# Kernel tuning notes

Hardware: AMD Instinct MI355X
Metric: run time of the kernel (lower is better)

## Reference

```python
import jax, jax.numpy as jnp
import numpy as np

N_FEAT = 350; D = 512; L = 4; DS = 64; NREG = 6; REG_E = 32
B = 32; S = 2048
CLAMP = 20.0


def _ln(x, g, b, eps=1e-5):
    mu = jnp.mean(x, axis=-1, keepdims=True)
    var = jnp.mean(jnp.square(x - mu), axis=-1, keepdims=True)
    return (x - mu) * jax.lax.rsqrt(var + eps) * g + b


def _slstm(x, ln_g, ln_b, Wi, bi, Wf, bf, Wz, bz, Wo, bo, Wp, bp):
    # x: [B,S,D] -> out: [B,S,D]
    xn = _ln(x, ln_g, ln_b)
    log_i = jnp.clip(jnp.einsum('bsd,de->bse', xn, Wi) + bi, -CLAMP, CLAMP)
    log_f = jnp.clip(jnp.einsum('bsd,de->bse', xn, Wf) + bf, -CLAMP, CLAMP)
    z = jnp.tanh(jnp.einsum('bsd,de->bse', xn, Wz) + bz)
    o = jax.nn.sigmoid(jnp.einsum('bsd,de->bse', xn, Wo) + bo)

    def step(carry, inp):
        m, c = carry
        li, lf, zt, ot = inp
        m_new = jnp.maximum(m + lf, li)
        i_s = jnp.exp(li - m_new)
        f_s = jnp.exp(m + lf - m_new)
        c_new = f_s * c + i_s * zt
        h = ot * jnp.tanh(c_new)
        return (m_new, c_new), h

    bsz = x.shape[0]
    init = (jnp.zeros((bsz, DS), x.dtype), jnp.zeros((bsz, DS), x.dtype))
    seq = (jnp.swapaxes(log_i, 0, 1), jnp.swapaxes(log_f, 0, 1),
           jnp.swapaxes(z, 0, 1), jnp.swapaxes(o, 0, 1))
    _, hs = jax.lax.scan(step, init, seq)  # hs: [S,B,DS]
    hs = jnp.swapaxes(hs, 0, 1)  # [B,S,DS]
    return jnp.einsum('bse,ed->bsd', hs, Wp) + bp


def setup_inputs() -> dict:
    key = jax.random.key(0)
    ks = iter(jax.random.split(key, 64))
    def p(*shape):
        return jax.random.normal(next(ks), shape, dtype=jnp.float32) * 0.02
    return {
        'x': jax.random.normal(next(ks), (B, S, N_FEAT), dtype=jnp.float32),
        'regime_ids': jax.random.randint(next(ks), (B, S), 0, NREG),
        'emb_regime': p(NREG, REG_E),
        'grn_w1': p(N_FEAT + REG_E, D), 'grn_b1': jnp.zeros((D,), jnp.float32),
        'grn_w2': p(D, N_FEAT), 'grn_b2': jnp.zeros((N_FEAT,), jnp.float32),
        'in_w': p(N_FEAT, D), 'in_b': jnp.zeros((D,), jnp.float32),
        'ln_in_g': jnp.ones((L, D), jnp.float32), 'ln_in_b': jnp.zeros((L, D), jnp.float32),
        'wi': p(L, D, DS), 'bi': jnp.zeros((L, DS), jnp.float32),
        'wf': p(L, D, DS), 'bf': jnp.zeros((L, DS), jnp.float32),
        'wz': p(L, D, DS), 'bz': jnp.zeros((L, DS), jnp.float32),
        'wo': p(L, D, DS), 'bo': jnp.zeros((L, DS), jnp.float32),
        'wp': p(L, DS, D), 'bp': jnp.zeros((L, D), jnp.float32),
        'nm_g': jnp.ones((L, D), jnp.float32), 'nm_b': jnp.zeros((L, D), jnp.float32),
        'hd15_w': p(D, 1), 'hd15_b': jnp.zeros((1,), jnp.float32),
        'hd30_w': p(D, 1), 'hd30_b': jnp.zeros((1,), jnp.float32),
        'hv_w': p(D, 3), 'hv_b': jnp.zeros((3,), jnp.float32),
        'hreg_w': p(D, NREG), 'hreg_b': jnp.zeros((NREG,), jnp.float32),
        'hrng_w': p(D, 3), 'hrng_b': jnp.zeros((3,), jnp.float32),
    }


def reference(x, regime_ids, emb_regime, grn_w1, grn_b1, grn_w2, grn_b2,
              in_w, in_b, ln_in_g, ln_in_b, wi, bi, wf, bf, wz, bz, wo, bo,
              wp, bp, nm_g, nm_b, hd15_w, hd15_b, hd30_w, hd30_b,
              hv_w, hv_b, hreg_w, hreg_b, hrng_w, hrng_b):
    # Variable selection network (regime-conditioned feature weights)
    remb = emb_regime[regime_ids]                      # [B,S,32]
    comb = jnp.concatenate([x, remb], axis=-1)         # [B,S,382]
    hidden = jax.nn.elu(jnp.einsum('bsf,fd->bsd', comb, grn_w1) + grn_b1)
    weights = jax.nn.softmax(jnp.einsum('bsd,df->bsf', hidden, grn_w2) + grn_b2, axis=-1)
    xw = x * weights
    h = jnp.einsum('bsf,fd->bsd', xw, in_w) + in_b     # [B,S,D]
    for l in range(L):
        res = _slstm(h, ln_in_g[l], ln_in_b[l], wi[l], bi[l], wf[l], bf[l],
                     wz[l], bz[l], wo[l], bo[l], wp[l], bp[l])
        h = _ln(h + res, nm_g[l], nm_b[l])
    h_last = h[:, -1, :]
    return (jnp.squeeze(h_last @ hd15_w + hd15_b, -1),
            jnp.squeeze(h_last @ hd30_w + hd30_b, -1),
            h_last @ hv_w + hv_b,
            h_last @ hreg_w + hreg_b,
            h_last @ hrng_w + hrng_b,
            h_last,
            weights[:, -1, :])
```

## Files before the change

kernel.cpp:

```cpp
#include <hip/hip_runtime.h>
#include <cmath>

#define NFEAT 350
#define DMODEL 512
#define NLAYER 4
#define DSZ 64
#define REG_E 32
#define BATCH 32
#define SEQ 2048
#define MTOK (BATCH * SEQ)
#define CLAMP_V 20.0f

#define CHUNK 64
#define NCHUNK (SEQ / CHUNK)

typedef short bf16x8 __attribute__((ext_vector_type(8)));
typedef float f32x4 __attribute__((ext_vector_type(4)));

__device__ __forceinline__ unsigned short f2b(float v) {
    union { float f; unsigned int u; } x; x.f = v;
    unsigned int r = x.u + 0x7fffu + ((x.u >> 16) & 1u);
    return (unsigned short)(r >> 16);
}
__device__ __forceinline__ float b2f(unsigned short u) {
    union { unsigned int i; float f; } x; x.i = ((unsigned int)u) << 16;
    return x.f;
}
__device__ __forceinline__ unsigned int pack2(float a, float b) {
    return ((unsigned int)f2b(b) << 16) | f2b(a);
}

__global__ __launch_bounds__(256) void tconv_k(const float* __restrict__ src,
                                               unsigned short* __restrict__ dst,
                                               int K, int N, int Kpad) {
    int k = blockIdx.x * 256 + threadIdx.x;
    int n = blockIdx.y;
    if (k >= Kpad) return;
    float v = (k < K && n < N) ? src[(size_t)k * N + n] : 0.f;
    dst[(size_t)n * Kpad + k] = f2b(v);
}

__global__ __launch_bounds__(256) void tconv_g_k(const float* __restrict__ wi,
                                                 const float* __restrict__ wf,
                                                 const float* __restrict__ wz,
                                                 const float* __restrict__ wo,
                                                 unsigned short* __restrict__ dst) {
    int k = blockIdx.x * 256 + threadIdx.x;
    int n = blockIdx.y;
    int z = blockIdx.z;
    int l = z >> 2, g = z & 3;
    const float* src = (g == 0 ? wi : g == 1 ? wf : g == 2 ? wz : wo) + (size_t)l * DMODEL * DSZ;
    dst[(size_t)z * 32768 + (size_t)n * 512 + k] = f2b(src[(size_t)k * DSZ + n]);
}

__global__ __launch_bounds__(1024) void gbias_k(const float* bi, const float* bf_,
                                                const float* bz, const float* bo,
                                                float* __restrict__ gbias) {
    int t = threadIdx.x;
    int l = t >> 8, r = t & 255, g = r >> 6, e = r & 63;
    const float* s = (g == 0 ? bi : g == 1 ? bf_ : g == 2 ? bz : bo);
    gbias[t] = s[l * 64 + e];
}

__global__ __launch_bounds__(256) void build_xc_k(const float* __restrict__ x,
                                                  const int* __restrict__ rid,
                                                  const float* __restrict__ emb,
                                                  unsigned short* __restrict__ xc) {
    int i = blockIdx.x * 256 + threadIdx.x;
    int m = i / 192, p = i - m * 192;
    int k = p * 2;
    float a = 0.f, b = 0.f;
    if (k < 350) {
        const float2 v = *(const float2*)(x + (size_t)m * NFEAT + k);
        a = v.x; b = v.y;
    } else if (k < 382) {
        int r = rid[m];
        const float2 v = *(const float2*)(emb + r * REG_E + (k - 350));
        a = v.x; b = v.y;
    }
    ((unsigned int*)xc)[(size_t)m * 192 + p] = pack2(a, b);
}

template <int ALD, int EPI>
__global__ __launch_bounds__(256) void mgemm_k(const unsigned short* __restrict__ Ab,
                                               const float* __restrict__ Af,
                                               const unsigned short* __restrict__ Bt,
                                               const float* __restrict__ bias,
                                               float* __restrict__ Cf,
                                               unsigned short* __restrict__ Cb,
                                               const float* __restrict__ muA,
                                               const float* __restrict__ rstdA,
                                               const float* __restrict__ lng,
                                               const float* __restrict__ lnb,
                                               float* __restrict__ statS,
                                               float* __restrict__ statQ,
                                               int lda, int ldb, int K, int N, int ldc) {
    __shared__ unsigned short As[128][40];
    __shared__ unsigned short Bs[128][40];
    const int tid = threadIdx.x;
    const int lane = tid & 63;
    const int wave = tid >> 6;
    const int l15 = lane & 15;
    const int quad = lane >> 4;
    const int wm = (wave >> 1) * 64;
    const int wn = (wave & 1) * 64;
    const size_t m0 = (size_t)blockIdx.y * 128;
    const int n0 = blockIdx.x * 128;

    const int sr = tid >> 2;
    const int ku = tid & 3;

    const unsigned short* Br0 = Bt + ((size_t)(n0 + sr)) * ldb + ku * 8;
    const unsigned short* Br1 = Br0 + (size_t)64 * ldb;

    const unsigned short* Ar0 = nullptr;
    const unsigned short* Ar1 = nullptr;
    const float* Fr0 = nullptr;
    const float* Fr1 = nullptr;
    float mu0 = 0.f, rs0 = 0.f, mu1 = 0.f, rs1 = 0.f;
    if (ALD == 0) {
        Ar0 = Ab + (m0 + sr) * (size_t)lda + ku * 8;
        Ar1 = Ar0 + (size_t)64 * lda;
    } else {
        Fr0 = Af + (m0 + sr) * (size_t)lda + ku * 8;
        Fr1 = Fr0 + (size_t)64 * lda;
        mu0 = muA[m0 + sr];   rs0 = rstdA[m0 + sr];
        mu1 = muA[m0 + sr + 64]; rs1 = rstdA[m0 + sr + 64];
    }

    f32x4 acc[4][4] = {};

    for (int k0 = 0; k0 < K; k0 += 32) {
        if (ALD == 0) {
            *(uint4*)&As[sr][ku * 8]      = *(const uint4*)(Ar0 + k0);
            *(uint4*)&As[sr + 64][ku * 8] = *(const uint4*)(Ar1 + k0);
        } else {
            float4 g0 = *(const float4*)(lng + k0 + ku * 8);
            float4 g1 = *(const float4*)(lng + k0 + ku * 8 + 4);
            float4 c0 = *(const float4*)(lnb + k0 + ku * 8);
            float4 c1 = *(const float4*)(lnb + k0 + ku * 8 + 4);
            {
                float4 v0 = *(const float4*)(Fr0 + k0);
                float4 v1 = *(const float4*)(Fr0 + k0 + 4);
                uint4 w;
                w.x = pack2((v0.x - mu0) * rs0 * g0.x + c0.x, (v0.y - mu0) * rs0 * g0.y + c0.y);
                w.y = pack2((v0.z - mu0) * rs0 * g0.z + c0.z, (v0.w - mu0) * rs0 * g0.w + c0.w);
                w.z = pack2((v1.x - mu0) * rs0 * g1.x + c1.x, (v1.y - mu0) * rs0 * g1.y + c1.y);
                w.w = pack2((v1.z - mu0) * rs0 * g1.z + c1.z, (v1.w - mu0) * rs0 * g1.w + c1.w);
                *(uint4*)&As[sr][ku * 8] = w;
            }
            {
                float4 v0 = *(const float4*)(Fr1 + k0);
                float4 v1 = *(const float4*)(Fr1 + k0 + 4);
                uint4 w;
                w.x = pack2((v0.x - mu1) * rs1 * g0.x + c0.x, (v0.y - mu1) * rs1 * g0.y + c0.y);
                w.y = pack2((v0.z - mu1) * rs1 * g0.z + c0.z, (v0.w - mu1) * rs1 * g0.w + c0.w);
                w.z = pack2((v1.x - mu1) * rs1 * g1.x + c1.x, (v1.y - mu1) * rs1 * g1.y + c1.y);
                w.w = pack2((v1.z - mu1) * rs1 * g1.z + c1.z, (v1.w - mu1) * rs1 * g1.w + c1.w);
                *(uint4*)&As[sr + 64][ku * 8] = w;
            }
        }
        *(uint4*)&Bs[sr][ku * 8]      = *(const uint4*)(Br0 + k0);
        *(uint4*)&Bs[sr + 64][ku * 8] = *(const uint4*)(Br1 + k0);
        __syncthreads();
        bf16x8 af[4], bf[4];
#pragma unroll
        for (int mt = 0; mt < 4; mt++)
            af[mt] = *(const bf16x8*)&As[wm + mt * 16 + l15][quad * 8];
#pragma unroll
        for (int nt = 0; nt < 4; nt++)
            bf[nt] = *(const bf16x8*)&Bs[wn + nt * 16 + l15][quad * 8];
#pragma unroll
        for (int mt = 0; mt < 4; mt++)
#pragma unroll
            for (int nt = 0; nt < 4; nt++)
                acc[mt][nt] = __builtin_amdgcn_mfma_f32_16x16x32_bf16(af[mt], bf[nt], acc[mt][nt], 0, 0, 0);
        __syncthreads();
    }

    float sA[4][4] = {}, qA[4][4] = {};

#pragma unroll
    for (int mt = 0; mt < 4; mt++) {
        int gmb = wm + mt * 16 + quad * 4;
#pragma unroll
        for (int nt = 0; nt < 4; nt++) {
            int gn = n0 + wn + nt * 16 + l15;
            if (gn < N) {
                float bv = bias[gn];
#pragma unroll
                for (int r = 0; r < 4; r++) {
                    size_t gm = m0 + gmb + r;
                    float v = acc[mt][nt][r] + bv;
                    if (EPI == 0) {
                        v = v > 0.f ? v : expm1f(v);
                        Cb[gm * (size_t)ldc + gn] = f2b(v);
                    } else if (EPI == 1) {
                        Cb[gm * (size_t)ldc + gn] = f2b(v);
                    } else if (EPI == 2) {
                        int g = gn >> 6;
                        if (g < 2) v = fminf(fmaxf(v, -CLAMP_V), CLAMP_V);
                        else if (g == 2) v = tanhf(v);
                        else v = 1.f / (1.f + expf(-v));
                        Cf[gm * (size_t)ldc + gn] = v;
                    } else {
                        Cf[gm * (size_t)ldc + gn] = v;
                        sA[mt][r] += v;
                        qA[mt][r] += v * v;
                    }
                }
            }
        }
    }

    if (EPI == 3 && statS != nullptr) {
#pragma unroll
        for (int mt = 0; mt < 4; mt++)
#pragma unroll
            for (int r = 0; r < 4; r++) {
                float s = sA[mt][r], q = qA[mt][r];
#pragma unroll
                for (int o = 1; o < 16; o <<= 1) {
                    s += __shfl_xor(s, o, 64);
                    q += __shfl_xor(q, o, 64);
                }
                if (l15 == 0) {
                    size_t gm = m0 + wm + mt * 16 + quad * 4 + r;
                    atomicAdd(&statS[gm], s);
                    atomicAdd(&statQ[gm], q);
                }
            }
    }
}

__global__ __launch_bounds__(256) void ln_fin_k(const float* __restrict__ statS,
                                                const float* __restrict__ statQ,
                                                float* __restrict__ mu,
                                                float* __restrict__ rstd) {
    int tok = blockIdx.x * 256 + threadIdx.x;
    float s = statS[tok], q = statQ[tok];
    float m = s * (1.f / DMODEL);
    float v = q * (1.f / DMODEL) - m * m;
    mu[tok] = m;
    rstd[tok] = rsqrtf(v + 1e-5f);
}

__global__ __launch_bounds__(256) void softmax_xw_k(const unsigned short* __restrict__ logits,
                                                    unsigned short* __restrict__ xc,
                                                    float* __restrict__ out_wlast) {
    int tok = blockIdx.x * 4 + (threadIdx.x >> 6);
    int lane = threadIdx.x & 63;
    const unsigned short* lr = logits + (size_t)tok * NFEAT;
    unsigned short* xr = xc + (size_t)tok * 384;
    float v[6];
    float mx = -1e30f;
#pragma unroll
    for (int i = 0; i < 6; i++) {
        int idx = lane + 64 * i;
        v[i] = (idx < NFEAT) ? b2f(lr[idx]) : -1e30f;
        mx = fmaxf(mx, v[i]);
    }
#pragma unroll
    for (int o = 32; o > 0; o >>= 1) mx = fmaxf(mx, __shfl_xor(mx, o, 64));
    float s = 0.f;
#pragma unroll
    for (int i = 0; i < 6; i++) { v[i] = expf(v[i] - mx); s += v[i]; }
#pragma unroll
    for (int o = 32; o > 0; o >>= 1) s += __shfl_xor(s, o, 64);
    float inv = 1.f / s;
    bool last = ((tok & (SEQ - 1)) == SEQ - 1);
    int b = tok >> 11;
#pragma unroll
    for (int i = 0; i < 6; i++) {
        int idx = lane + 64 * i;
        if (idx < NFEAT) {
            float w = v[i] * inv;
            xr[idx] = f2b(w * b2f(xr[idx]));
            if (last) out_wlast[b * NFEAT + idx] = w;
        } else if (idx < 352) {
            xr[idx] = 0;
        }
    }
}

__global__ __launch_bounds__(256) void seg_agg_k(const float* __restrict__ gates,
                                                 float* __restrict__ aggF,
                                                 float* __restrict__ aggL,
                                                 float* __restrict__ aggS) {
    int b = blockIdx.x >> 3;
    int cg = blockIdx.x & 7;
    int chunk = cg * 4 + (threadIdx.x >> 6);
    int e = threadIdx.x & 63;
    const float* gp = gates + ((size_t)b * SEQ + (size_t)chunk * CHUNK) * 256;
    float F = 0.f, L = -1e30f, s = 0.f;
#pragma unroll 4
    for (int t = 0; t < CHUNK; t++) {
        const float* q = gp + (size_t)t * 256;
        float li = q[e], lf = q[64 + e], z = q[128 + e];
        float Ln = fmaxf(L + lf, li);
        s = expf(L + lf - Ln) * s + expf(li - Ln) * z;
        L = Ln;
        F += lf;
    }
    int idx = (b * NCHUNK + chunk) * 64 + e;
    aggF[idx] = F; aggL[idx] = L; aggS[idx] = s;
}

__global__ __launch_bounds__(64) void chunk_scan_k(const float* __restrict__ aggF,
                                                   const float* __restrict__ aggL,
                                                   const float* __restrict__ aggS,
                                                   float* __restrict__ stM,
                                                   float* __restrict__ stC) {
    int b = blockIdx.x;
    int e = threadIdx.x;
    float F[NCHUNK], L[NCHUNK], S[NCHUNK];
#pragma unroll
    for (int k = 0; k < NCHUNK; k++) {
        int idx = (b * NCHUNK + k) * 64 + e;
        F[k] = aggF[idx];
        L[k] = aggL[idx];
        S[k] = aggS[idx];
    }
    float m = 0.f, c = 0.f;
#pragma unroll
    for (int k = 0; k < NCHUNK; k++) {
        int idx = (b * NCHUNK + k) * 64 + e;
        stM[idx] = m; stC[idx] = c;
        float mn = fmaxf(m + F[k], L[k]);
        c = expf(m + F[k] - mn) * c + expf(L[k] - mn) * S[k];
        m = mn;
    }
}

__global__ __launch_bounds__(256) void replay_k(const float* __restrict__ gates,
                                                const float* __restrict__ stM,
                                                const float* __restrict__ stC,
                                                float* __restrict__ hs) {
    int b = blockIdx.x >> 3;
    int cg = blockIdx.x & 7;
    int chunk = cg * 4 + (threadIdx.x >> 6);
    int e = threadIdx.x & 63;
    int s0 = chunk * CHUNK;
    const float* gp = gates + ((size_t)b * SEQ + s0) * 256;
    float* hp = hs + ((size_t)b * SEQ + s0) * DSZ;
    int idx = (b * NCHUNK + chunk) * 64 + e;
    float m = stM[idx], c = stC[idx];
#pragma unroll 4
    for (int t = 0; t < CHUNK; t++) {
        const float* q = gp + (size_t)t * 256;
        float li = q[e], lf = q[64 + e], z = q[128 + e], o = q[192 + e];
        float mlf = m + lf;
        float mn = fmaxf(mlf, li);
        c = expf(mlf - mn) * c + expf(li - mn) * z;
        m = mn;
        hp[(size_t)t * DSZ + e] = o * tanhf(c);
    }
}

__global__ __launch_bounds__(256) void outproj_k(const float* __restrict__ hs,
                                                 const float* __restrict__ wp,
                                                 const float* __restrict__ bp,
                                                 const float* __restrict__ nmg,
                                                 const float* __restrict__ nmb,
                                                 float* __restrict__ h,
                                                 float* __restrict__ mu,
                                                 float* __restrict__ rstd) {
    __shared__ float shs[32][DSZ];
    __shared__ float swp[16][DMODEL];
    int wv = threadIdx.x >> 6;
    int lane = threadIdx.x & 63;
    int tok0 = blockIdx.x * 32;

    {
        const float4* src = (const float4*)(hs + (size_t)tok0 * DSZ);
        float4* dst = (float4*)&shs[0][0];
        dst[threadIdx.x] = src[threadIdx.x];
        dst[threadIdx.x + 256] = src[threadIdx.x + 256];
    }
    __syncthreads();

    float acc[8][8] = {};
    for (int k0 = 0; k0 < DSZ; k0 += 16) {
        const float4* src = (const float4*)(wp + (size_t)k0 * DMODEL);
#pragma unroll
        for (int i = 0; i < 8; i++)
            ((float4*)&swp[0][0])[threadIdx.x + i * 256] = src[threadIdx.x + i * 256];
        __syncthreads();
#pragma unroll
        for (int k = 0; k < 16; k++) {
            float bv[8];
#pragma unroll
            for (int j = 0; j < 8; j++) bv[j] = swp[k][lane + 64 * j];
#pragma unroll
            for (int t = 0; t < 8; t++) {
                float av = shs[wv * 8 + t][k0 + k];
#pragma unroll
                for (int j = 0; j < 8; j++) acc[t][j] += av * bv[j];
            }
        }
        __syncthreads();
    }

#pragma unroll
    for (int t = 0; t < 8; t++) {
        int tok = tok0 + wv * 8 + t;
        float u[8];
        float s = 0.f, sq = 0.f;
#pragma unroll
        for (int j = 0; j < 8; j++) {
            int col = lane + 64 * j;
            float v = h[(size_t)tok * DMODEL + col] + acc[t][j] + bp[col];
            u[j] = v;
            s += v; sq += v * v;
        }
#pragma unroll
        for (int o = 32; o > 0; o >>= 1) { s += __shfl_xor(s, o, 64); sq += __shfl_xor(sq, o, 64); }
        float mean = s * (1.f / DMODEL);
        float var = sq * (1.f / DMODEL) - mean * mean;
        float rs = rsqrtf(var + 1e-5f);
        float s2 = 0.f, sq2 = 0.f;
#pragma unroll
        for (int j = 0; j < 8; j++) {
            int col = lane + 64 * j;
            float v = (u[j] - mean) * rs * nmg[col] + nmb[col];
            h[(size_t)tok * DMODEL + col] = v;
            s2 += v; sq2 += v * v;
        }
#pragma unroll
        for (int o = 32; o > 0; o >>= 1) { s2 += __shfl_xor(s2, o, 64); sq2 += __shfl_xor(sq2, o, 64); }
        if (lane == 0) {
            float m2 = s2 * (1.f / DMODEL);
            float v2 = sq2 * (1.f / DMODEL) - m2 * m2;
            mu[tok] = m2;
            rstd[tok] = rsqrtf(v2 + 1e-5f);
        }
    }
}

__global__ __launch_bounds__(64) void heads_k(const float* __restrict__ h,
                                              const float* hd15_w, const float* hd15_b,
                                              const float* hd30_w, const float* hd30_b,
                                              const float* hv_w, const float* hv_b,
                                              const float* hreg_w, const float* hreg_b,
                                              const float* hrng_w, const float* hrng_b,
                                              float* __restrict__ out) {
    int b = blockIdx.x;
    int lane = threadIdx.x;
    __shared__ float row[DMODEL];
    const float* hp = h + (size_t)(b * SEQ + SEQ - 1) * DMODEL;
#pragma unroll
    for (int i = 0; i < 8; i++) row[lane + 64 * i] = hp[lane + 64 * i];
    __syncthreads();
#pragma unroll
    for (int i = 0; i < 8; i++) out[448 + b * DMODEL + lane + 64 * i] = row[lane + 64 * i];
    if (lane < 14) {
        const float* w; const float* bb;
        int ncol, j, off;
        if (lane == 0)      { w = hd15_w; bb = hd15_b; ncol = 1; j = 0;         off = 0 + b; }
        else if (lane == 1) { w = hd30_w; bb = hd30_b; ncol = 1; j = 0;         off = 32 + b; }
        else if (lane < 5)  { j = lane - 2;  w = hv_w;   bb = hv_b;   ncol = 3; off = 64 + b * 3 + j; }
        else if (lane < 11) { j = lane - 5;  w = hreg_w; bb = hreg_b; ncol = 6; off = 160 + b * 6 + j; }
        else                { j = lane - 11; w = hrng_w; bb = hrng_b; ncol = 3; off = 352 + b * 3 + j; }
        float s = bb[j];
        for (int k = 0; k < DMODEL; k++) s += row[k] * w[k * ncol + j];
        out[off] = s;
    }
}

extern "C" void kernel_launch(void* const* d_in, const int* in_sizes, int n_in,
                              void* d_out, int out_size, void* d_ws, size_t ws_size,
                              hipStream_t stream) {
    (void)in_sizes; (void)n_in; (void)out_size; (void)ws_size;
    const float* x      = (const float*)d_in[0];
    const int*   rid    = (const int*)d_in[1];
    const float* emb    = (const float*)d_in[2];
    const float* grn_w1 = (const float*)d_in[3];
    const float* grn_b1 = (const float*)d_in[4];
    const float* grn_w2 = (const float*)d_in[5];
    const float* grn_b2 = (const float*)d_in[6];
    const float* in_w   = (const float*)d_in[7];
    const float* in_b   = (const float*)d_in[8];
    const float* ln_g   = (const float*)d_in[9];
    const float* ln_b   = (const float*)d_in[10];
    const float* wi     = (const float*)d_in[11];
    const float* bi     = (const float*)d_in[12];
    const float* wf     = (const float*)d_in[13];
    const float* bf_    = (const float*)d_in[14];
    const float* wz     = (const float*)d_in[15];
    const float* bz     = (const float*)d_in[16];
    const float* wo     = (const float*)d_in[17];
    const float* bo     = (const float*)d_in[18];
    const float* wp     = (const float*)d_in[19];
    const float* bp     = (const float*)d_in[20];
    const float* nm_g   = (const float*)d_in[21];
    const float* nm_b   = (const float*)d_in[22];

    float* out = (float*)d_out;
    char* W = (char*)d_ws;

    float* h               = (float*)W;
    unsigned short* hidden = (unsigned short*)W;
    unsigned short* logits = (unsigned short*)(W + 67108864);
    char* RB = W + 134217728;
    unsigned short* xc = (unsigned short*)RB;
    float* gates  = (float*)RB;
    float* hsbuf  = (float*)(RB + 67108864);
    char* RM = W + 218103808;
    float* aggF  = (float*)(RM);
    float* aggL  = (float*)(RM + 262144);
    float* aggS  = (float*)(RM + 524288);
    float* stM   = (float*)(RM + 786432);
    float* stC   = (float*)(RM + 1048576);
    float* mu    = (float*)(RM + 1310720);
    float* rstd  = (float*)(RM + 1572864);
    unsigned short* w1t  = (unsigned short*)(RM + 1835008);
    unsigned short* w2t  = (unsigned short*)(RM + 2228224);
    unsigned short* inwt = (unsigned short*)(RM + 2621440);
    unsigned short* gwt  = (unsigned short*)(RM + 2981888);
    float* gbias         = (float*)(RM + 4030464);
    float* statS         = (float*)(RM + 4034560);
    float* statQ         = (float*)(RM + 4296704);

    build_xc_k<<<MTOK * 192 / 256, 256, 0, stream>>>(x, rid, emb, xc);
    tconv_k<<<dim3(2, 512), 256, 0, stream>>>(grn_w1, w1t, 382, 512, 384);
    tconv_k<<<dim3(2, 384), 256, 0, stream>>>(grn_w2, w2t, 512, 350, 512);
    tconv_k<<<dim3(2, 512), 256, 0, stream>>>(in_w, inwt, 350, 512, 352);
    tconv_g_k<<<dim3(2, 64, 16), 256, 0, stream>>>(wi, wf, wz, wo, gwt);
    gbias_k<<<1, 1024, 0, stream>>>(bi, bf_, bz, bo, gbias);
    hipMemsetAsync(statS, 0, 262144, stream);
    hipMemsetAsync(statQ, 0, 262144, stream);

    mgemm_k<0, 0><<<dim3(4, 512), 256, 0, stream>>>(xc, nullptr, w1t, grn_b1, nullptr, hidden,
                                                    nullptr, nullptr, nullptr, nullptr,
                                                    nullptr, nullptr,
                                                    384, 384, 384, 512, 512);
    mgemm_k<0, 1><<<dim3(3, 512), 256, 0, stream>>>(hidden, nullptr, w2t, grn_b2, nullptr, logits,
                                                    nullptr, nullptr, nullptr, nullptr,
                                                    nullptr, nullptr,
                                                    512, 512, 512, 350, 350);
    softmax_xw_k<<<MTOK / 4, 256, 0, stream>>>(logits, xc, out + 16832);
    mgemm_k<0, 3><<<dim3(4, 512), 256, 0, stream>>>(xc, nullptr, inwt, in_b, h, nullptr,
                                                    nullptr, nullptr, nullptr, nullptr,
                                                    statS, statQ,
                                                    384, 352, 352, 512, 512);
    ln_fin_k<<<MTOK / 256, 256, 0, stream>>>(statS, statQ, mu, rstd);

    for (int l = 0; l < NLAYER; l++) {
        mgemm_k<1, 2><<<dim3(2, 512), 256, 0, stream>>>(nullptr, h, gwt + (size_t)l * 131072,
                                                        gbias + l * 256, gates, nullptr,
                                                        mu, rstd,
                                                        ln_g + l * DMODEL, ln_b + l * DMODEL,
                                                        nullptr, nullptr,
                                                        512, 512, 512, 256, 256);
        seg_agg_k<<<BATCH * 8, 256, 0, stream>>>(gates, aggF, aggL, aggS);
        chunk_scan_k<<<BATCH, 64, 0, stream>>>(aggF, aggL, aggS, stM, stC);
        replay_k<<<BATCH * 8, 256, 0, stream>>>(gates, stM, stC, hsbuf);

        outproj_k<<<MTOK / 32, 256, 0, stream>>>(hsbuf,
                                                 wp + (size_t)l * DSZ * DMODEL,
                                                 bp + l * DMODEL,
                                                 nm_g + l * DMODEL,
                                                 nm_b + l * DMODEL,
                                                 h, mu, rstd);
    }

    heads_k<<<BATCH, 64, 0, stream>>>(h,
                                      (const float*)d_in[23], (const float*)d_in[24],
                                      (const float*)d_in[25], (const float*)d_in[26],
                                      (const float*)d_in[27], (const float*)d_in[28],
                                      (const float*)d_in[29], (const float*)d_in[30],
                                      (const float*)d_in[31], (const float*)d_in[32],
                                      out);
}
```

Measured before the change: 1.293 ms.

## Use split-bf16 MFMA for sLSTM output projection with fused residual LayerNorm

Replaces the FP32 scalar-FMA output projection (64->512 per token) with an MFMA kernel. Both the hidden states and the projection weights are stored as bf16 hi/lo pairs, and three bf16 MFMA products (hi*hi, lo*hi, hi*lo) recover near-FP32 accuracy. The replay kernel now writes the hi/lo bf16 pairs directly, and a new prep kernel transposes and splits the weights. This removes the LDS-staged scalar GEMM, at the cost of three times the MFMA work and a different LayerNorm reduction layout that goes through shared memory across waves.

New measurement: 1.376 ms. 1.06x slower.

```diff
diff --git a/kernel.cpp b/kernel.cpp
--- a/kernel.cpp
+++ b/kernel.cpp
@@ -38,6 +38,21 @@
     if (k >= Kpad) return;
     float v = (k < K && n < N) ? src[(size_t)k * N + n] : 0.f;
     dst[(size_t)n * Kpad + k] = f2b(v);
+}
+
+__global__ __launch_bounds__(256) void tconv_wp_k(const float* __restrict__ wp,
+                                                  unsigned short* __restrict__ dst) {
+    int idx = blockIdx.x * 256 + threadIdx.x;
+    int l = idx >> 15;
+    int rem = idx & 32767;
+    int n = rem >> 6;
+    int k = rem & 63;
+    float v = wp[((size_t)l * 64 + k) * 512 + n];
+    unsigned short hi = f2b(v);
+    unsigned short lo = f2b(v - b2f(hi));
+    unsigned short* d = dst + ((size_t)l * 512 + n) * 128;
+    d[k] = hi;
+    d[64 + k] = lo;
 }
 
 __global__ __launch_bounds__(256) void tconv_g_k(const float* __restrict__ wi,
@@ -335,14 +350,14 @@
 __global__ __launch_bounds__(256) void replay_k(const float* __restrict__ gates,
                                                 const float* __restrict__ stM,
                                                 const float* __restrict__ stC,
-                                                float* __restrict__ hs) {
+                                                unsigned short* __restrict__ hs) {
     int b = blockIdx.x >> 3;
     int cg = blockIdx.x & 7;
     int chunk = cg * 4 + (threadIdx.x >> 6);
     int e = threadIdx.x & 63;
     int s0 = chunk * CHUNK;
     const float* gp = gates + ((size_t)b * SEQ + s0) * 256;
-    float* hp = hs + ((size_t)b * SEQ + s0) * DSZ;
+    unsigned short* hp = hs + ((size_t)b * SEQ + s0) * 128;
     int idx = (b * NCHUNK + chunk) * 64 + e;
     float m = stM[idx], c = stC[idx];
 #pragma unroll 4
@@ -353,87 +368,106 @@
         float mn = fmaxf(mlf, li);
         c = expf(mlf - mn) * c + expf(li - mn) * z;
         m = mn;
-        hp[(size_t)t * DSZ + e] = o * tanhf(c);
-    }
-}
-
-__global__ __launch_bounds__(256) void outproj_k(const float* __restrict__ hs,
-                                                 const float* __restrict__ wp,
-                                                 const float* __restrict__ bp,
-                                                 const float* __restrict__ nmg,
-                                                 const float* __restrict__ nmb,
-                                                 float* __restrict__ h,
-                                                 float* __restrict__ mu,
-                                                 float* __restrict__ rstd) {
-    __shared__ float shs[32][DSZ];
-    __shared__ float swp[16][DMODEL];
-    int wv = threadIdx.x >> 6;
-    int lane = threadIdx.x & 63;
-    int tok0 = blockIdx.x * 32;
-
-    {
-        const float4* src = (const float4*)(hs + (size_t)tok0 * DSZ);
-        float4* dst = (float4*)&shs[0][0];
-        dst[threadIdx.x] = src[threadIdx.x];
-        dst[threadIdx.x + 256] = src[threadIdx.x + 256];
-    }
+        float v = o * tanhf(c);
+        unsigned short hi = f2b(v);
+        hp[(size_t)t * 128 + e] = hi;
+        hp[(size_t)t * 128 + 64 + e] = f2b(v - b2f(hi));
+    }
+}
+
+__global__ __launch_bounds__(256) void outproj_mfma_k(const unsigned short* __restrict__ hs,
+                                                      const unsigned short* __restrict__ wpt,
+                                                      const float* __restrict__ bp,
+                                                      const float* __restrict__ nmg,
+                                                      const float* __restrict__ nmb,
+                                                      float* __restrict__ h,
+                                                      float* __restrict__ mu,
+                                                      float* __restrict__ rstd) {
+    __shared__ float sS[16][4], sQ[16][4], sS2[16][4], sQ2[16][4];
+    const int tid = threadIdx.x;
+    const int lane = tid & 63;
+    const int wv = tid >> 6;
+    const int l15 = lane & 15;
+    const int quad = lane >> 4;
+    const size_t tok0 = (size_t)blockIdx.x * 16;
+
+    const unsigned short* hr = hs + (tok0 + l15) * 128;
+    bf16x8 b_hi0 = *(const bf16x8*)(hr + quad * 8);
+    bf16x8 b_hi1 = *(const bf16x8*)(hr + 32 + quad * 8);
+    bf16x8 b_lo0 = *(const bf16x8*)(hr + 64 + quad * 8);
+    bf16x8 b_lo1 = *(const bf16x8*)(hr + 96 + quad * 8);
+
+    f32x4 acc[8];
+    const unsigned short* wbase = wpt + (size_t)(wv * 128 + l15) * 128 + quad * 8;
+#pragma unroll
+    for (int mt = 0; mt < 8; mt++) {
+        const unsigned short* wa = wbase + (size_t)mt * 16 * 128;
+        bf16x8 a_hi0 = *(const bf16x8*)(wa);
+        bf16x8 a_hi1 = *(const bf16x8*)(wa + 32);
+        bf16x8 a_lo0 = *(const bf16x8*)(wa + 64);
+        bf16x8 a_lo1 = *(const bf16x8*)(wa + 96);
+        f32x4 a = {};
+        a = __builtin_amdgcn_mfma_f32_16x16x32_bf16(a_hi0, b_hi0, a, 0, 0, 0);
+        a = __builtin_amdgcn_mfma_f32_16x16x32_bf16(a_hi1, b_hi1, a, 0, 0, 0);
+        a = __builtin_amdgcn_mfma_f32_16x16x32_bf16(a_lo0, b_hi0, a, 0, 0, 0);
+        a = __builtin_amdgcn_mfma_f32_16x16x32_bf16(a_lo1, b_hi1, a, 0, 0, 0);
+        a = __builtin_amdgcn_mfma_f32_16x16x32_bf16(a_hi0, b_lo0, a, 0, 0, 0);
+        a = __builtin_amdgcn_mfma_f32_16x16x32_bf16(a_hi1, b_lo1, a, 0, 0, 0);
+        acc[mt] = a;
+    }
+
+    const size_t hoff = (tok0 + l15) * (size_t)DMODEL;
+
+    float s = 0.f, sq = 0.f;
+#pragma unroll
+    for (int mt = 0; mt < 8; mt++) {
+        int col = wv * 128 + mt * 16 + quad * 4;
+        float4 hv = *(const float4*)(h + hoff + col);
+        float4 bv = *(const float4*)(bp + col);
+        acc[mt][0] += hv.x + bv.x;
+        acc[mt][1] += hv.y + bv.y;
+        acc[mt][2] += hv.z + bv.z;
+        acc[mt][3] += hv.w + bv.w;
+        s += acc[mt][0] + acc[mt][1] + acc[mt][2] + acc[mt][3];
+        sq += acc[mt][0] * acc[mt][0] + acc[mt][1] * acc[mt][1]
+            + acc[mt][2] * acc[mt][2] + acc[mt][3] * acc[mt][3];
+    }
+    s += __shfl_xor(s, 16, 64); sq += __shfl_xor(sq, 16, 64);
+    s += __shfl_xor(s, 32, 64); sq += __shfl_xor(sq, 32, 64);
+    if (lane < 16) { sS[l15][wv] = s; sQ[l15][wv] = sq; }
     __syncthreads();
-
-    float acc[8][8] = {};
-    for (int k0 = 0; k0 < DSZ; k0 += 16) {
-        const float4* src = (const float4*)(wp + (size_t)k0 * DMODEL);
-#pragma unroll
-        for (int i = 0; i < 8; i++)
-            ((float4*)&swp[0][0])[threadIdx.x + i * 256] = src[threadIdx.x + i * 256];
-        __syncthreads();
-#pragma unroll
-        for (int k = 0; k < 16; k++) {
-            float bv[8];
-#pragma unroll
-            for (int j = 0; j < 8; j++) bv[j] = swp[k][lane + 64 * j];
-#pragma unroll
-            for (int t = 0; t < 8; t++) {
-                float av = shs[wv * 8 + t][k0 + k];
-#pragma unroll
-                for (int j = 0; j < 8; j++) acc[t][j] += av * bv[j];
-            }
-        }
-        __syncthreads();
-    }
-
-#pragma unroll
-    for (int t = 0; t < 8; t++) {
-        int tok = tok0 + wv * 8 + t;
-        float u[8];
-        float s = 0.f, sq = 0.f;
-#pragma unroll
-        for (int j = 0; j < 8; j++) {
-            int col = lane + 64 * j;
-            float v = h[(size_t)tok * DMODEL + col] + acc[t][j] + bp[col];
-            u[j] = v;
-            s += v; sq += v * v;
-        }
-#pragma unroll
-        for (int o = 32; o > 0; o >>= 1) { s += __shfl_xor(s, o, 64); sq += __shfl_xor(sq, o, 64); }
-        float mean = s * (1.f / DMODEL);
-        float var = sq * (1.f / DMODEL) - mean * mean;
-        float rs = rsqrtf(var + 1e-5f);
-        float s2 = 0.f, sq2 = 0.f;
-#pragma unroll
-        for (int j = 0; j < 8; j++) {
-            int col = lane + 64 * j;
-            float v = (u[j] - mean) * rs * nmg[col] + nmb[col];
-            h[(size_t)tok * DMODEL + col] = v;
-            s2 += v; sq2 += v * v;
-        }
-#pragma unroll
-        for (int o = 32; o > 0; o >>= 1) { s2 += __shfl_xor(s2, o, 64); sq2 += __shfl_xor(sq2, o, 64); }
-        if (lane == 0) {
-            float m2 = s2 * (1.f / DMODEL);
-            float v2 = sq2 * (1.f / DMODEL) - m2 * m2;
-            mu[tok] = m2;
-            rstd[tok] = rsqrtf(v2 + 1e-5f);
-        }
+    float S = sS[l15][0] + sS[l15][1] + sS[l15][2] + sS[l15][3];
+    float Q = sQ[l15][0] + sQ[l15][1] + sQ[l15][2] + sQ[l15][3];
+    float mean = S * (1.f / DMODEL);
+    float var = Q * (1.f / DMODEL) - mean * mean;
+    float rs = rsqrtf(var + 1e-5f);
+
+    float s2 = 0.f, sq2 = 0.f;
+#pragma unroll
+    for (int mt = 0; mt < 8; mt++) {
+        int col = wv * 128 + mt * 16 + quad * 4;
+        float4 gv = *(const float4*)(nmg + col);
+        float4 bbv = *(const float4*)(nmb + col);
+        float4 v;
+        v.x = (acc[mt][0] - mean) * rs * gv.x + bbv.x;
+        v.y = (acc[mt][1] - mean) * rs * gv.y + bbv.y;
+        v.z = (acc[mt][2] - mean) * rs * gv.z + bbv.z;
+        v.w = (acc[mt][3] - mean) * rs * gv.w + bbv.w;
+        *(float4*)(h + hoff + col) = v;
+        s2 += v.x + v.y + v.z + v.w;
+        sq2 += v.x * v.x + v.y * v.y + v.z * v.z + v.w * v.w;
+    }
+    s2 += __shfl_xor(s2, 16, 64); sq2 += __shfl_xor(sq2, 16, 64);
+    s2 += __shfl_xor(s2, 32, 64); sq2 += __shfl_xor(sq2, 32, 64);
+    if (lane < 16) { sS2[l15][wv] = s2; sQ2[l15][wv] = sq2; }
+    __syncthreads();
+    if (tid < 16) {
+        float S2 = sS2[tid][0] + sS2[tid][1] + sS2[tid][2] + sS2[tid][3];
+        float Q2 = sQ2[tid][0] + sQ2[tid][1] + sQ2[tid][2] + sQ2[tid][3];
+        float m2 = S2 * (1.f / DMODEL);
+        float v2 = Q2 * (1.f / DMODEL) - m2 * m2;
+        mu[tok0 + tid] = m2;
+        rstd[tok0 + tid] = rsqrtf(v2 + 1e-5f);
     }
 }
 
@@ -504,7 +538,7 @@
     char* RB = W + 134217728;
     unsigned short* xc = (unsigned short*)RB;
     float* gates  = (float*)RB;
-    float* hsbuf  = (float*)(RB + 67108864);
+    unsigned short* hsbuf = (unsigned short*)(RB + 67108864);
     char* RM = W + 218103808;
     float* aggF  = (float*)(RM);
     float* aggL  = (float*)(RM + 262144);
@@ -520,6 +554,7 @@
     float* gbias         = (float*)(RM + 4030464);
     float* statS         = (float*)(RM + 4034560);
     float* statQ         = (float*)(RM + 4296704);
+    unsigned short* wpt  = (unsigned short*)(RM + 4558848);
 
     build_xc_k<<<MTOK * 192 / 256, 256, 0, stream>>>(x, rid, emb, xc);
     tconv_k<<<dim3(2, 512), 256, 0, stream>>>(grn_w1, w1t, 382, 512, 384);
@@ -527,6 +562,7 @@
     tconv_k<<<dim3(2, 512), 256, 0, stream>>>(in_w, inwt, 350, 512, 352);
     tconv_g_k<<<dim3(2, 64, 16), 256, 0, stream>>>(wi, wf, wz, wo, gwt);
     gbias_k<<<1, 1024, 0, stream>>>(bi, bf_, bz, bo, gbias);
+    tconv_wp_k<<<512, 256, 0, stream>>>(wp, wpt);
     hipMemsetAsync(statS, 0, 262144, stream);
     hipMemsetAsync(statQ, 0, 262144, stream);
 
@@ -556,12 +592,12 @@
         chunk_scan_k<<<BATCH, 64, 0, stream>>>(aggF, aggL, aggS, stM, stC);
         replay_k<<<BATCH * 8, 256, 0, stream>>>(gates, stM, stC, hsbuf);
 
-        outproj_k<<<MTOK / 32, 256, 0, stream>>>(hsbuf,
-                                                 wp + (size_t)l * DSZ * DMODEL,
-                                                 bp + l * DMODEL,
-                                                 nm_g + l * DMODEL,
-                                                 nm_b + l * DMODEL,
-                                                 h, mu, rstd);
+        outproj_mfma_k<<<MTOK / 16, 256, 0, stream>>>(hsbuf,
+                                                      wpt + (size_t)l * 65536,
+                                                      bp + l * DMODEL,
+                                                      nm_g + l * DMODEL,
+                                                      nm_b + l * DMODEL,
+                                                      h, mu, rstd);
     }
 
     heads_k<<<BATCH, 64, 0, stream>>>(h,
```
